# Kernel tuning notes

Hardware: AMD Instinct MI355X
Metric: run time of the kernel (lower is better)

The kernel has to match this reference:

```python
import jax, jax.numpy as jnp
import numpy as np

# Config constants (match init_kwargs)
V, E, DQ, DM, S = 50257, 256, 128, 256, 8192
WLOC, KR, KW, O = 64, 8, 4, 256
DECAY = 0.99
B, T = 8, 32


def setup_inputs() -> dict:
    key = jax.random.key(0)
    ks = jax.random.split(key, 24)
    def w(k, shape, s=0.05):
        return jax.random.normal(k, shape, jnp.float32) * s
    return {
        "input_ids": jax.random.randint(ks[0], (B, T), 0, V, dtype=jnp.int32),
        "embedding": w(ks[1], (V, E), 0.02),
        "Wq": w(ks[2], (E, DQ)), "Wk": w(ks[3], (E, DQ)), "Wv": w(ks[4], (E, E)),
        "Wr": w(ks[5], (3 * E, DM)),
        "Wx0": w(ks[6], (2 * E, 2 * E)), "Wh0": w(ks[7], (E, 2 * E)), "b0": jnp.zeros((2 * E,), jnp.float32),
        "Wx1": w(ks[8], (E, 2 * E)), "Wh1": w(ks[9], (E, 2 * E)), "b1": jnp.zeros((2 * E,), jnp.float32),
        "Wx2": w(ks[10], (E, 2 * E)), "Wh2": w(ks[11], (E, 2 * E)), "b2": jnp.zeros((2 * E,), jnp.float32),
        "Ww": w(ks[12], (3 * E, DM)), "Wwq": w(ks[13], (3 * E, DM)),
        "ln_g": jnp.ones((3 * E,), jnp.float32), "ln_b": jnp.zeros((3 * E,), jnp.float32),
        "Wout": w(ks[14], (3 * E, O)), "bout": jnp.zeros((O,), jnp.float32),
        "memory_init": jnp.zeros((B, S, DM), jnp.float32),
    }


def _tier(x, s, Wx, Wh, b):
    # GRU-style gated update: pre -> (update gate z, candidate h)
    pre = x @ Wx + s @ Wh + b
    z, h = jnp.split(pre, 2, axis=-1)
    z = jax.nn.sigmoid(z)
    return (1.0 - z) * s + z * jnp.tanh(h)


def reference(input_ids, embedding, Wq, Wk, Wv, Wr,
              Wx0, Wh0, b0, Wx1, Wh1, b1, Wx2, Wh2, b2,
              Ww, Wwq, ln_g, ln_b, Wout, bout, memory_init):
    Bsz = input_ids.shape[0]
    inv_sq_dq = 1.0 / np.sqrt(DQ).astype(np.float32)
    inv_sq_dm = 1.0 / np.sqrt(DM).astype(np.float32)

    def step(carry, tok):
        mem, rema, lw, s0, s1, s2, buf, t = carry
        e = embedding[tok]                                    # [B,E]
        # --- local sliding-window attention (circular buffer + validity mask) ---
        valid = jnp.minimum(t, WLOC)
        q = e @ Wq                                            # [B,DQ]
        k = buf @ Wk                                          # [B,W,DQ]
        v = buf @ Wv                                          # [B,W,E]
        sc = jnp.einsum('bwd,bd->bw', k, q) * inv_sq_dq
        mask = jnp.arange(WLOC) < valid
        sc = jnp.where(mask[None, :], sc, -1e9)
        attn = jax.nn.softmax(sc, axis=-1)
        local_read = jnp.einsum('bw,bwd->bd', attn, v) * (valid > 0).astype(e.dtype)
        buf = buf.at[:, t % WLOC, :].set(e)                   # update buffer
        # --- sparse top-k router read from memory bank ---
        u = jnp.concatenate([e, s0, s2], axis=-1)             # [B,3E]
        qm = u @ Wr                                           # [B,DM]
        rsc = jnp.einsum('bsd,bd->bs', mem, qm) * inv_sq_dm - 0.1 * rema
        rvals, ridx = jax.lax.top_k(rsc, KR)
        alpha = jax.nn.softmax(rvals, axis=-1)                # [B,KR]
        rows = jnp.take_along_axis(mem, ridx[:, :, None], axis=1)
        r = jnp.einsum('bk,bkd->bd', alpha, rows)             # [B,DM]
        rema = DECAY * rema
        rema = jax.vmap(lambda rr, ii, aa: rr.at[ii].add(aa))(rema, ridx, alpha)
        # --- hierarchical tier update (period-gated) ---
        x0 = jnp.concatenate([e, r + local_read], axis=-1)
        s0n = _tier(x0, s0, Wx0, Wh0, b0)                     # period 1
        s1n = jnp.where(t % 2 == 0, _tier(s0n, s1, Wx1, Wh1, b1), s1)
        s2n = jnp.where(t % 4 == 0, _tier(s1n, s2, Wx2, Wh2, b2), s2)
        # --- memory writer: gated scatter write to top-k stale/underused slots ---
        u2 = jnp.concatenate([s0n, s2n, r], axis=-1)          # [B,3E]
        wvec = jnp.tanh(u2 @ Ww)                              # [B,DM]
        qw = u2 @ Wwq
        tf = t.astype(jnp.float32)
        stale = (tf - lw.astype(jnp.float32)) / (tf + 1.0)
        under = 1.0 / (1.0 + rema)
        wsc = jnp.einsum('bsd,bd->bs', mem, qw) * inv_sq_dm + 0.5 * stale + 0.5 * under
        gvals, widx = jax.lax.top_k(wsc, KW)
        g = jax.nn.sigmoid(gvals)[..., None]                  # [B,KW,1]
        old = jnp.take_along_axis(mem, widx[:, :, None], axis=1)
        newrows = (1.0 - g) * old + g * wvec[:, None, :]
        mem = jax.vmap(lambda m, i, vv: m.at[i].set(vv))(mem, widx, newrows)
        lw = jax.vmap(lambda l, i: l.at[i].set(t))(lw, widx)
        # --- layernorm over concatenated tiers + output head ---
        cat = jnp.concatenate([s0n, s1n, s2n], axis=-1)       # [B,3E]
        mu = cat.mean(-1, keepdims=True)
        var = ((cat - mu) ** 2).mean(-1, keepdims=True)
        nrm = (cat - mu) / jnp.sqrt(var + 1e-5) * ln_g + ln_b
        logits = nrm @ Wout + bout
        return (mem, rema, lw, s0n, s1n, s2n, buf, t + 1), logits

    init = (memory_init,
            jnp.zeros((Bsz, S), jnp.float32),
            jnp.zeros((Bsz, S), jnp.int32),
            jnp.zeros((Bsz, E), jnp.float32),
            jnp.zeros((Bsz, E), jnp.float32),
            jnp.zeros((Bsz, E), jnp.float32),
            jnp.zeros((Bsz, WLOC, E), jnp.float32),
            jnp.int32(0))
    _, logits = jax.lax.scan(step, init, input_ids.T)         # [T,B,O]
    return jnp.transpose(logits, (1, 0, 2))                   # [B,T,O]
```

## Files before the change

### kernel.cpp

```cpp
#include <hip/hip_runtime.h>
#include <math.h>

static constexpr int Bz = 8;
static constexpr int Tn = 32;
static constexpr int Ed = 256;
static constexpr int Dm = 256;
static constexpr int Sn = 8192;
static constexpr int Kr = 8;
static constexpr int Kw = 4;

#define INV_SQ_DQ 0.08838834764831845f
#define INV_SQ_DM 0.0625f
#define DECAYF    0.99f
#define LD4(p) (*reinterpret_cast<const float4*>(p))

__device__ __forceinline__ float wsc_formula(float aw, float tf, float lwf, float inv_t1, float rm) {
  return aw + 0.5f * ((tf - lwf) * inv_t1) + 0.5f / (1.f + rm);
}

template<int RA, int RB>
__device__ __forceinline__ void gseg(const float* __restrict__ W, const float* __restrict__ xv,
                                     int j4, float4& acc) {
#pragma unroll 16
  for (int r = RA; r < RB; ++r) {
    float4 w4 = LD4(W + (size_t)r * 512 + j4);
    float x = xv[r];
    acc.x += x * w4.x; acc.y += x * w4.y; acc.z += x * w4.z; acc.w += x * w4.w;
  }
}

__device__ __forceinline__ void first_untouched(const int* __restrict__ flagb, int K, int tid,
                                                int* un, int* ucnt, int* wcnt) {
  if (tid == 0) *ucnt = 0;
  __syncthreads();
  for (int chunk = 0; chunk < 2; ++chunk) {
    int idx = chunk * 256 + tid;
    bool pred = (flagb[idx] == 0);
    unsigned long long m = __ballot(pred);
    int lane = tid & 63, wv = tid >> 6;
    if (lane == 0) wcnt[wv] = __popcll(m);
    __syncthreads();
    int pre = *ucnt;
    for (int w2 = 0; w2 < wv; ++w2) pre += wcnt[w2];
    pre += __popcll(m & ((1ull << lane) - 1ull));
    if (pred && pre < K) un[pre] = idx;
    __syncthreads();
    if (tid == 0) {
      int tot = wcnt[0] + wcnt[1] + wcnt[2] + wcnt[3];
      int nc = *ucnt + tot; *ucnt = nc > K ? K : nc;
    }
    __syncthreads();
  }
}

__device__ __forceinline__ void topk_sel(const float* __restrict__ cv, const int* __restrict__ cs,
                                         int n, int K, int tid, float* tv, int* ts,
                                         float* rv, int* ri) {
  float v0 = (tid < n) ? cv[tid] : -INFINITY;        int s0 = (tid < n) ? cs[tid] : 0x7fffffff;
  float v1 = (tid + 256 < n) ? cv[tid + 256] : -INFINITY; int s1 = (tid + 256 < n) ? cs[tid + 256] : 0x7fffffff;
  float v2 = (tid + 512 < n) ? cv[tid + 512] : -INFINITY; int s2 = (tid + 512 < n) ? cs[tid + 512] : 0x7fffffff;
  int lane = tid & 63, wv = tid >> 6;
  for (int k = 0; k < K; ++k) {
    float bv = v0; int bs = s0;
    if (v1 > bv || (v1 == bv && s1 < bs)) { bv = v1; bs = s1; }
    if (v2 > bv || (v2 == bv && s2 < bs)) { bv = v2; bs = s2; }
    for (int off = 32; off; off >>= 1) {
      float ov = __shfl_down(bv, off); int os = __shfl_down(bs, off);
      if (ov > bv || (ov == bv && os < bs)) { bv = ov; bs = os; }
    }
    if (lane == 0) { rv[wv] = bv; ri[wv] = bs; }
    __syncthreads();
    if (tid == 0) {
      float gv = rv[0]; int gs = ri[0];
      for (int w = 1; w < 4; ++w) if (rv[w] > gv || (rv[w] == gv && ri[w] < gs)) { gv = rv[w]; gs = ri[w]; }
      tv[k] = gv; ts[k] = gs;
    }
    __syncthreads();
    int gs = ts[k];
    if (s0 == gs) v0 = -INFINITY;
    if (s1 == gs) v1 = -INFINITY;
    if (s2 == gs) v2 = -INFINITY;
  }
}

__global__ __launch_bounds__(256) void k_pre1(
    const int* __restrict__ ids, const float* __restrict__ emb,
    const float* __restrict__ Wk, const float* __restrict__ Wq, const float* __restrict__ Wv,
    float* __restrict__ Kpre, float* __restrict__ qpre, float* __restrict__ Vpre) {
  int bt = blockIdx.x, tid = threadIdx.x;
  int b = bt >> 5, tt = bt & 31;
  __shared__ float el[256];
  el[tid] = emb[(size_t)ids[b * Tn + tt] * Ed + tid];
  __syncthreads();
  float a = 0.f;
  if (tid < 128) {
#pragma unroll 8
    for (int d = 0; d < 256; ++d) a += el[d] * Wk[d * 128 + tid];
    Kpre[(size_t)bt * 128 + tid] = a;
  } else {
    int j = tid - 128;
#pragma unroll 8
    for (int d = 0; d < 256; ++d) a += el[d] * Wq[d * 128 + j];
    qpre[(size_t)bt * 128 + j] = a;
  }
  float av = 0.f;
#pragma unroll 8
  for (int d = 0; d < 256; ++d) av += el[d] * Wv[d * 256 + tid];
  Vpre[(size_t)bt * 256 + tid] = av;
}

__global__ __launch_bounds__(256) void k_pre2(
    const float* __restrict__ Kpre, const float* __restrict__ qpre, const float* __restrict__ Vpre,
    float* __restrict__ lrpre) {
  int bt = blockIdx.x, tid = threadIdx.x;
  int b = bt >> 5, tt = bt & 31;
  if (tt == 0) { lrpre[(size_t)bt * 256 + tid] = 0.f; return; }
  __shared__ float ql[128];
  __shared__ float scl[32];
  __shared__ float attn_s[64];
  if (tid < 128) ql[tid] = qpre[(size_t)bt * 128 + tid];
  __syncthreads();
  int w = tid >> 3, i = tid & 7;
  float p = 0.f;
  if (w < tt) {
    const float* kp = Kpre + (size_t)(b * Tn + w) * 128 + i * 16;
    const float* qp = ql + i * 16;
#pragma unroll
    for (int d = 0; d < 16; ++d) p += kp[d] * qp[d];
  }
  p += __shfl_xor(p, 1); p += __shfl_xor(p, 2); p += __shfl_xor(p, 4);
  if (i == 0 && w < tt) scl[w] = p * INV_SQ_DQ;
  __syncthreads();
  if (tid < 64) {
    float val = (tid < tt) ? scl[tid] : -INFINITY;
    float m = val;
    for (int off = 32; off; off >>= 1) m = fmaxf(m, __shfl_xor(m, off));
    float ex = (tid < tt) ? expf(val - m) : 0.f;
    float sm = ex;
    for (int off = 32; off; off >>= 1) sm += __shfl_xor(sm, off);
    attn_s[tid] = ex / sm;
  }
  __syncthreads();
  float acc = 0.f;
  for (int w2 = 0; w2 < tt; ++w2) acc += attn_s[w2] * Vpre[(size_t)(b * Tn + w2) * 256 + tid];
  lrpre[(size_t)bt * 256 + tid] = acc;
}

__global__ __launch_bounds__(256) void k_read(
    const float* __restrict__ rsc, float* __restrict__ rema, const float* __restrict__ mem,
    float* __restrict__ rbuf, int* __restrict__ flagI, int* __restrict__ listI,
    int* __restrict__ countI) {
  int b = blockIdx.x, tid = threadIdx.x;
  int* flagb = flagI + b * Sn;
  int* listb = listI + b * 512;
  const float* rscb = rsc + (size_t)b * Sn;
  float* remab = rema + (size_t)b * Sn;
  int cnt = countI[b];
  __shared__ float cv[544]; __shared__ int cs[544];
  __shared__ int un[8]; __shared__ int ucnt; __shared__ int wcnt[4];
  __shared__ float rv[4]; __shared__ int ri[4];
  __shared__ float tv[Kr]; __shared__ int ts[Kr];
  for (int i = tid; i < cnt; i += 256) { int s = listb[i]; cv[i] = rscb[s]; cs[i] = s; }
  first_untouched(flagb, Kr, tid, un, &ucnt, wcnt);
  if (tid < Kr) { cv[cnt + tid] = 0.f; cs[cnt + tid] = un[tid]; }
  __syncthreads();
  topk_sel(cv, cs, cnt + Kr, Kr, tid, tv, ts, rv, ri);
  float mx = tv[0];
  float ssum = 0.f;
#pragma unroll
  for (int k = 0; k < Kr; ++k) ssum += expf(tv[k] - mx);
  float inv = 1.f / ssum;
  float racc = 0.f;
#pragma unroll
  for (int k = 0; k < Kr; ++k)
    racc += (expf(tv[k] - mx) * inv) * mem[((size_t)b * Sn + ts[k]) * 256 + tid];
  rbuf[b * 256 + tid] = racc;
  for (int i = tid; i < cnt; i += 256) remab[listb[i]] *= DECAYF;
  __syncthreads();
  if (tid < Kr) {
    int s = ts[tid];
    remab[s] += expf(tv[tid] - mx) * inv;
    if (flagb[s] == 0) { flagb[s] = 1; int pos = atomicAdd(&countI[b], 1); listb[pos] = s; }
  }
}

__global__ __launch_bounds__(512) void k_tiers(
    const int* __restrict__ ids, const float* __restrict__ emb,
    const float* __restrict__ lrpre, const float* __restrict__ rbuf,
    const float* __restrict__ Wx0, const float* __restrict__ Wh0, const float* __restrict__ b0v,
    const float* __restrict__ Wx1, const float* __restrict__ Wh1, const float* __restrict__ b1v,
    const float* __restrict__ Wx2, const float* __restrict__ Wh2, const float* __restrict__ b2v,
    float* __restrict__ s0g, float* __restrict__ s1g, float* __restrict__ s2g, int t) {
  int b = blockIdx.x, tid = threadIdx.x;
  __shared__ float xa[768];
  __shared__ float snl[256];
  __shared__ float sold[256];
  __shared__ float part[4][512];
  if (tid < 256) {
    xa[tid] = emb[(size_t)ids[b * Tn + t] * Ed + tid];
    xa[512 + tid] = s0g[b * 256 + tid];
  } else {
    int d = tid - 256;
    xa[256 + d] = rbuf[b * 256 + d] + lrpre[(size_t)(b * Tn + t) * 256 + d];
  }
  __syncthreads();
  int quar = tid >> 7;
  int j4 = (tid & 127) << 2;
  {
    float4 acc = {0.f, 0.f, 0.f, 0.f};
    if (quar == 0)      gseg<0, 192>(Wx0, xa, j4, acc);
    else if (quar == 1) gseg<192, 384>(Wx0, xa, j4, acc);
    else if (quar == 2) { gseg<384, 512>(Wx0, xa, j4, acc); gseg<0, 64>(Wh0, xa + 512, j4, acc); }
    else                gseg<64, 256>(Wh0, xa + 512, j4, acc);
    *reinterpret_cast<float4*>(&part[quar][j4]) = acc;
  }
  __syncthreads();
  if (tid < 256) {
    float z = part[0][tid] + part[1][tid] + part[2][tid] + part[3][tid] + b0v[tid];
    float h = part[0][tid + 256] + part[1][tid + 256] + part[2][tid + 256] + part[3][tid + 256] + b0v[tid + 256];
    float zz = 1.f / (1.f + expf(-z));
    float ns = (1.f - zz) * xa[512 + tid] + zz * tanhf(h);
    s0g[b * 256 + tid] = ns; snl[tid] = ns;
  }
  __syncthreads();
  if ((t & 1) == 0) {
    if (tid < 256) sold[tid] = s1g[b * 256 + tid];
    __syncthreads();
    {
      float4 acc = {0.f, 0.f, 0.f, 0.f};
      if (quar == 0)      gseg<0, 128>(Wx1, snl, j4, acc);
      else if (quar == 1) gseg<128, 256>(Wx1, snl, j4, acc);
      else if (quar == 2) gseg<0, 128>(Wh1, sold, j4, acc);
      else                gseg<128, 256>(Wh1, sold, j4, acc);
      *reinterpret_cast<float4*>(&part[quar][j4]) = acc;
    }
    __syncthreads();
    if (tid < 256) {
      float z = part[0][tid] + part[1][tid] + part[2][tid] + part[3][tid] + b1v[tid];
      float h = part[0][tid + 256] + part[1][tid + 256] + part[2][tid + 256] + part[3][tid + 256] + b1v[tid + 256];
      float zz = 1.f / (1.f + expf(-z));
      float ns = (1.f - zz) * sold[tid] + zz * tanhf(h);
      s1g[b * 256 + tid] = ns;
    }
    __syncthreads();
    if ((t & 3) == 0) {
      if (tid < 256) { snl[tid] = s1g[b * 256 + tid]; sold[tid] = s2g[b * 256 + tid]; }
      __syncthreads();
      {
        float4 acc = {0.f, 0.f, 0.f, 0.f};
        if (quar == 0)      gseg<0, 128>(Wx2, snl, j4, acc);
        else if (quar == 1) gseg<128, 256>(Wx2, snl, j4, acc);
        else if (quar == 2) gseg<0, 128>(Wh2, sold, j4, acc);
        else                gseg<128, 256>(Wh2, sold, j4, acc);
        *reinterpret_cast<float4*>(&part[quar][j4]) = acc;
      }
      __syncthreads();
      if (tid < 256) {
        float z = part[0][tid] + part[1][tid] + part[2][tid] + part[3][tid] + b2v[tid];
        float h = part[0][tid + 256] + part[1][tid + 256] + part[2][tid + 256] + part[3][tid + 256] + b2v[tid + 256];
        float zz = 1.f / (1.f + expf(-z));
        s2g[b * 256 + tid] = (1.f - zz) * sold[tid] + zz * tanhf(h);
      }
    }
  }
}

__global__ __launch_bounds__(256) void k_midp(
    const int* __restrict__ ids, const float* __restrict__ emb,
    const float* __restrict__ Wr, const float* __restrict__ Wwq, const float* __restrict__ Ww,
    const float* __restrict__ s0g, const float* __restrict__ s1g, const float* __restrict__ s2g,
    const float* __restrict__ rbuf,
    const float* __restrict__ lng, const float* __restrict__ lnb,
    float* __restrict__ qmP, float* __restrict__ qwP, float* __restrict__ wvP,
    float* __restrict__ nrm, int t) {
  int wg = blockIdx.x, tid = threadIdx.x;
  if (wg < 96) {
    int m = wg >> 5;
    int r = wg & 31;
    int b = r >> 2, q = r & 3;
    if (m == 0 && t + 1 >= Tn) return;
    if (m != 0 && t >= Tn - 1) return;
    __shared__ float xl[192];
    if (tid < 192) {
      int row = q * 192 + tid;
      float val;
      if (m == 0) {
        if (row < 256) val = emb[(size_t)ids[b * Tn + t + 1] * Ed + row];
        else if (row < 512) val = s0g[b * 256 + row - 256];
        else val = s2g[b * 256 + row - 512];
      } else {
        if (row < 256) val = s0g[b * 256 + row];
        else if (row < 512) val = s2g[b * 256 + row - 256];
        else val = rbuf[b * 256 + row - 512];
      }
      xl[tid] = (m < 2) ? val * INV_SQ_DM : val;
    }
    __syncthreads();
    const float* W = (m == 0) ? Wr : (m == 1) ? Wwq : Ww;
    W += (size_t)(q * 192) * 256;
    float a = 0.f;
#pragma unroll 16
    for (int i = 0; i < 192; ++i) a += xl[i] * W[(size_t)i * 256 + tid];
    float* dst = (m == 0) ? qmP : (m == 1) ? qwP : wvP;
    dst[q * 2048 + b * 256 + tid] = a;
  } else {
    int b = wg - 96;
    __shared__ float red[4];
    float c0 = s0g[b * 256 + tid], c1 = s1g[b * 256 + tid], c2 = s2g[b * 256 + tid];
    float partl = c0 + c1 + c2;
    int lane = tid & 63, wv = tid >> 6;
    for (int off = 32; off; off >>= 1) partl += __shfl_down(partl, off);
    if (lane == 0) red[wv] = partl;
    __syncthreads();
    float mu = (red[0] + red[1] + red[2] + red[3]) * (1.f / 768.f);
    __syncthreads();
    float d0 = c0 - mu, d1 = c1 - mu, d2 = c2 - mu;
    float p2 = d0 * d0 + d1 * d1 + d2 * d2;
    for (int off = 32; off; off >>= 1) p2 += __shfl_down(p2, off);
    if (lane == 0) red[wv] = p2;
    __syncthreads();
    float var = (red[0] + red[1] + red[2] + red[3]) * (1.f / 768.f);
    float rstd = 1.f / sqrtf(var + 1e-5f);
    nrm[b * 768 + tid]       = d0 * rstd * lng[tid]       + lnb[tid];
    nrm[b * 768 + tid + 256] = d1 * rstd * lng[tid + 256] + lnb[tid + 256];
    nrm[b * 768 + tid + 512] = d2 * rstd * lng[tid + 512] + lnb[tid + 512];
  }
}

__global__ __launch_bounds__(256) void k_logits(
    const float* __restrict__ nrm, const float* __restrict__ Wout, const float* __restrict__ boutp,
    float* __restrict__ out, int t) {
  int wg = blockIdx.x, tid = threadIdx.x;
  int b = wg >> 2, c = wg & 3;
  __shared__ float lnl[192];
  if (tid < 192) lnl[tid] = nrm[b * 768 + c * 192 + tid];
  __syncthreads();
  float a = (c == 0) ? boutp[tid] : 0.f;
#pragma unroll 16
  for (int i = 0; i < 192; ++i) a += lnl[i] * Wout[(size_t)(c * 192 + i) * 256 + tid];
  atomicAdd(out + ((size_t)b * Tn + t) * 256 + tid, a);
}

__global__ __launch_bounds__(256) void k_scores(
    const float* __restrict__ mem, const float* __restrict__ qmP, const float* __restrict__ qwP,
    const float* __restrict__ rema, const int* __restrict__ lwI,
    const int* __restrict__ listI, const int* __restrict__ countI,
    float* __restrict__ rsc, float* __restrict__ wsc, int t) {
  int wg = blockIdx.x, tid = threadIdx.x;
  int b = wg >> 2, partq = wg & 3;
  int lane = tid & 63, wv = tid >> 6;
  int cnt = countI[b];
  float4 qm4 = {0, 0, 0, 0}, qw4 = {0, 0, 0, 0};
#pragma unroll
  for (int q = 0; q < 4; ++q) {
    float4 a = LD4(qmP + q * 2048 + b * 256 + lane * 4);
    float4 c = LD4(qwP + q * 2048 + b * 256 + lane * 4);
    qm4.x += a.x; qm4.y += a.y; qm4.z += a.z; qm4.w += a.w;
    qw4.x += c.x; qw4.y += c.y; qw4.z += c.z; qw4.w += c.w;
  }
  float tf = (float)t;
  float inv_t1 = 1.f / (tf + 1.f);
  for (int i = partq * 4 + wv; i < cnt; i += 16) {
    int s = listI[b * 512 + i];
    float4 m4 = LD4(mem + ((size_t)b * Sn + s) * 256 + lane * 4);
    float ar = m4.x * qm4.x + m4.y * qm4.y + m4.z * qm4.z + m4.w * qm4.w;
    float aw = m4.x * qw4.x + m4.y * qw4.y + m4.z * qw4.z + m4.w * qw4.w;
    for (int off = 32; off; off >>= 1) { ar += __shfl_down(ar, off); aw += __shfl_down(aw, off); }
    if (lane == 0) {
      float rm = rema[(size_t)b * Sn + s];
      float lwf = (float)lwI[b * Sn + s];
      rsc[(size_t)b * Sn + s] = ar - 0.1f * rm;
      wsc[(size_t)b * Sn + s] = wsc_formula(aw, tf, lwf, inv_t1, rm);
    }
  }
}

__global__ __launch_bounds__(256) void k_write(
    const float* __restrict__ wsc, float* __restrict__ mem,
    const float* __restrict__ wvP, const float* __restrict__ qmP,
    const float* __restrict__ rema, int* __restrict__ lwI,
    float* __restrict__ rsc, int* __restrict__ flagI, int* __restrict__ listI,
    int* __restrict__ countI, int t) {
  int b = blockIdx.x, tid = threadIdx.x;
  int* flagb = flagI + b * Sn;
  int* listb = listI + b * 512;
  const float* wscb = wsc + (size_t)b * Sn;
  float* rscb = rsc + (size_t)b * Sn;
  const float* remab = rema + (size_t)b * Sn;
  int cnt = countI[b];
  __shared__ float cv[544]; __shared__ int cs[544];
  __shared__ int un[8]; __shared__ int ucnt; __shared__ int wcnt[4];
  __shared__ float rv[4]; __shared__ int ri[4];
  __shared__ float tv[Kw]; __shared__ int ts[Kw];
  for (int i = tid; i < cnt; i += 256) { int s = listb[i]; cv[i] = wscb[s]; cs[i] = s; }
  first_untouched(flagb, Kw, tid, un, &ucnt, wcnt);
  float tf = (float)t;
  float inv_t1 = 1.f / (tf + 1.f);
  if (tid < Kw) { cv[cnt + tid] = wsc_formula(0.f, tf, 0.f, inv_t1, 0.f); cs[cnt + tid] = un[tid]; }
  __syncthreads();
  topk_sel(cv, cs, cnt + Kw, Kw, tid, tv, ts, rv, ri);
  float wvv = tanhf(wvP[0 * 2048 + b * 256 + tid] + wvP[1 * 2048 + b * 256 + tid] +
                    wvP[2 * 2048 + b * 256 + tid] + wvP[3 * 2048 + b * 256 + tid]);
  float qv = qmP[0 * 2048 + b * 256 + tid] + qmP[1 * 2048 + b * 256 + tid] +
             qmP[2 * 2048 + b * 256 + tid] + qmP[3 * 2048 + b * 256 + tid];
  int lane = tid & 63, wv = tid >> 6;
  for (int k = 0; k < Kw; ++k) {
    int s = ts[k];
    float g = 1.f / (1.f + expf(-tv[k]));
    float* row = mem + ((size_t)b * Sn + s) * 256;
    float nv = (1.f - g) * row[tid] + g * wvv;
    row[tid] = nv;
    float p = nv * qv;
    for (int off = 32; off; off >>= 1) p += __shfl_down(p, off);
    if (lane == 0) rv[wv] = p;
    __syncthreads();
    if (tid == 0) {
      rscb[s] = (rv[0] + rv[1] + rv[2] + rv[3]) - 0.1f * remab[s];
      lwI[b * Sn + s] = t;
    }
    __syncthreads();
  }
  if (tid < Kw) {
    int s = ts[tid];
    if (flagb[s] == 0) { flagb[s] = 1; int pos = atomicAdd(&countI[b], 1); listb[pos] = s; }
  }
}

extern "C" void kernel_launch(void* const* d_in, const int* in_sizes, int n_in,
                              void* d_out, int out_size, void* d_ws, size_t ws_size,
                              hipStream_t stream) {
  (void)in_sizes; (void)n_in; (void)out_size; (void)ws_size;
  const int*   ids   = (const int*)d_in[0];
  const float* emb   = (const float*)d_in[1];
  const float* Wq    = (const float*)d_in[2];
  const float* Wk    = (const float*)d_in[3];
  const float* Wv    = (const float*)d_in[4];
  const float* Wr    = (const float*)d_in[5];
  const float* Wx0   = (const float*)d_in[6];
  const float* Wh0   = (const float*)d_in[7];
  const float* b0p   = (const float*)d_in[8];
  const float* Wx1   = (const float*)d_in[9];
  const float* Wh1   = (const float*)d_in[10];
  const float* b1p   = (const float*)d_in[11];
  const float* Wx2   = (const float*)d_in[12];
  const float* Wh2   = (const float*)d_in[13];
  const float* b2p   = (const float*)d_in[14];
  const float* Ww    = (const float*)d_in[15];
  const float* Wwq   = (const float*)d_in[16];
  const float* lng   = (const float*)d_in[17];
  const float* lnb   = (const float*)d_in[18];
  const float* Wout  = (const float*)d_in[19];
  const float* boutp = (const float*)d_in[20];
  float* mem = (float*)d_in[21];

  float* ws = (float*)d_ws;
  size_t off = 0;
  float* rsc  = ws + off; off += (size_t)Bz * Sn;
  float* wsc  = ws + off; off += (size_t)Bz * Sn;
  float* rema = ws + off; off += (size_t)Bz * Sn;
  int*   lwI   = (int*)(ws + off); off += (size_t)Bz * Sn;
  int*   flagI = (int*)(ws + off); off += (size_t)Bz * Sn;
  int*   listI = (int*)(ws + off); off += (size_t)Bz * 512;
  int*   countI = (int*)(ws + off); off += 64;
  float* qmP  = ws + off; off += 4 * 2048;
  float* qwP  = ws + off; off += 4 * 2048;
  float* wvP  = ws + off; off += 4 * 2048;
  float* rbuf = ws + off; off += Bz * Ed;
  float* s0g  = ws + off; off += Bz * Ed;
  float* s1g  = ws + off; off += Bz * Ed;
  float* s2g  = ws + off; off += Bz * Ed;
  float* nrm  = ws + off; off += Bz * 768;
  float* Kpre = ws + off; off += (size_t)Bz * Tn * 128;
  float* qpre = ws + off; off += (size_t)Bz * Tn * 128;
  float* Vpre = ws + off; off += (size_t)Bz * Tn * 256;
  float* lrpre = ws + off; off += (size_t)Bz * Tn * 256;

  hipMemsetAsync(d_ws, 0, off * sizeof(float), stream);
  hipMemsetAsync(d_out, 0, (size_t)Bz * Tn * 256 * sizeof(float), stream);

  k_pre1<<<256, 256, 0, stream>>>(ids, emb, Wk, Wq, Wv, Kpre, qpre, Vpre);
  k_pre2<<<256, 256, 0, stream>>>(Kpre, qpre, Vpre, lrpre);

  for (int t = 0; t < Tn; ++t) {
    k_read<<<8, 256, 0, stream>>>(rsc, rema, mem, rbuf, flagI, listI, countI);
    k_tiers<<<8, 512, 0, stream>>>(ids, emb, lrpre, rbuf,
                                   Wx0, Wh0, b0p, Wx1, Wh1, b1p, Wx2, Wh2, b2p,
                                   s0g, s1g, s2g, t);
    k_midp<<<104, 256, 0, stream>>>(ids, emb, Wr, Wwq, Ww, s0g, s1g, s2g, rbuf,
                                    lng, lnb, qmP, qwP, wvP, nrm, t);
    k_logits<<<32, 256, 0, stream>>>(nrm, Wout, boutp, (float*)d_out, t);
    if (t < Tn - 1) {
      k_scores<<<32, 256, 0, stream>>>(mem, qmP, qwP, rema, lwI, listI, countI, rsc, wsc, t);
      k_write<<<8, 256, 0, stream>>>(wsc, mem, wvP, qmP, rema, lwI, rsc, flagI, listI, countI, t);
    }
  }
}
```

Baseline: 2.321 ms.

## Fuse per-step kernels into a persistent megakernel with grid barriers

Replaces the roughly 190 per-timestep kernel launches with one persistent kernel of 64 blocks that steps through phases separated by atomic-counter grid barriers. The tier GEMVs, projections and logits are split across more blocks with K-chunk partials reduced in a follow-up phase, and write plus next read are merged into one phase. Tier updates for s1 and s2 are gated on t parity, and the memset of d_out and several buffers is dropped. This targets launch overhead and latency on a serial recurrence, at the cost of spin-wait barriers that rely on all 64 blocks being co-resident.

```diff
diff --git a/kernel.cpp b/kernel.cpp
--- a/kernel.cpp
+++ b/kernel.cpp
@@ -1,85 +1,368 @@
 #include <hip/hip_runtime.h>
 #include <math.h>
 
-static constexpr int Bz = 8;
-static constexpr int Tn = 32;
-static constexpr int Ed = 256;
-static constexpr int Dm = 256;
-static constexpr int Sn = 8192;
-static constexpr int Kr = 8;
-static constexpr int Kw = 4;
-
+static constexpr int Bz = 8, Tn = 32, Sn = 8192, Kr = 8, Kw = 4;
 #define INV_SQ_DQ 0.08838834764831845f
 #define INV_SQ_DM 0.0625f
 #define DECAYF    0.99f
+#define NBLK      64
 #define LD4(p) (*reinterpret_cast<const float4*>(p))
 
-__device__ __forceinline__ float wsc_formula(float aw, float tf, float lwf, float inv_t1, float rm) {
-  return aw + 0.5f * ((tf - lwf) * inv_t1) + 0.5f / (1.f + rm);
-}
-
-template<int RA, int RB>
-__device__ __forceinline__ void gseg(const float* __restrict__ W, const float* __restrict__ xv,
-                                     int j4, float4& acc) {
-#pragma unroll 16
-  for (int r = RA; r < RB; ++r) {
-    float4 w4 = LD4(W + (size_t)r * 512 + j4);
-    float x = xv[r];
-    acc.x += x * w4.x; acc.y += x * w4.y; acc.z += x * w4.z; acc.w += x * w4.w;
-  }
-}
-
-__device__ __forceinline__ void first_untouched(const int* __restrict__ flagb, int K, int tid,
-                                                int* un, int* ucnt, int* wcnt) {
-  if (tid == 0) *ucnt = 0;
+struct MA {
+  const int* ids; const float* emb;
+  const float* Wr;
+  const float* Wx0; const float* Wh0; const float* b0;
+  const float* Wx1; const float* Wh1; const float* b1;
+  const float* Wx2; const float* Wh2; const float* b2;
+  const float* Ww; const float* Wwq; const float* lng; const float* lnb;
+  const float* Wout; const float* bout;
+  float* mem; float* out;
+  float* rsc; float* wsc; float* rema; int* lw; int* flag; int* list; int* cnt;
+  int* bar;
+  float* s0; float* s1; float* s2; float* rbuf; float* x0; float* nrm;
+  float* qmv; float* qwv; float* wvv;
+  float* pT; float* pP; float* pL;
+  const float* lrpre;
+};
+
+struct Sh {
+  float* xs; float* cv; int* cs; float* tv; int* ts; float* rv; int* ri;
+  int* un; int* uc; int* wc;
+};
+
+__device__ __forceinline__ void gbar(int* cnt, int ep) {
+  __syncthreads();
+  if (threadIdx.x == 0) {
+    __threadfence();
+    atomicAdd(cnt, 1);
+    int tgt = ep * NBLK;
+    while (__hip_atomic_load(cnt, __ATOMIC_RELAXED, __HIP_MEMORY_SCOPE_AGENT) < tgt)
+      __builtin_amdgcn_s_sleep(8);
+    __threadfence();
+  }
+  __syncthreads();
+}
+
+__device__ void first_untouched(const int* __restrict__ flagb, int K, int tid, const Sh& sh) {
+  if (tid == 0) *sh.uc = 0;
   __syncthreads();
   for (int chunk = 0; chunk < 2; ++chunk) {
     int idx = chunk * 256 + tid;
     bool pred = (flagb[idx] == 0);
     unsigned long long m = __ballot(pred);
     int lane = tid & 63, wv = tid >> 6;
-    if (lane == 0) wcnt[wv] = __popcll(m);
-    __syncthreads();
-    int pre = *ucnt;
-    for (int w2 = 0; w2 < wv; ++w2) pre += wcnt[w2];
+    if (lane == 0) sh.wc[wv] = __popcll(m);
+    __syncthreads();
+    int pre = *sh.uc;
+    for (int w2 = 0; w2 < wv; ++w2) pre += sh.wc[w2];
     pre += __popcll(m & ((1ull << lane) - 1ull));
-    if (pred && pre < K) un[pre] = idx;
+    if (pred && pre < K) sh.un[pre] = idx;
     __syncthreads();
     if (tid == 0) {
-      int tot = wcnt[0] + wcnt[1] + wcnt[2] + wcnt[3];
-      int nc = *ucnt + tot; *ucnt = nc > K ? K : nc;
-    }
-    __syncthreads();
-  }
-}
-
-__device__ __forceinline__ void topk_sel(const float* __restrict__ cv, const int* __restrict__ cs,
-                                         int n, int K, int tid, float* tv, int* ts,
-                                         float* rv, int* ri) {
-  float v0 = (tid < n) ? cv[tid] : -INFINITY;        int s0 = (tid < n) ? cs[tid] : 0x7fffffff;
-  float v1 = (tid + 256 < n) ? cv[tid + 256] : -INFINITY; int s1 = (tid + 256 < n) ? cs[tid + 256] : 0x7fffffff;
-  float v2 = (tid + 512 < n) ? cv[tid + 512] : -INFINITY; int s2 = (tid + 512 < n) ? cs[tid + 512] : 0x7fffffff;
+      int tot = sh.wc[0] + sh.wc[1] + sh.wc[2] + sh.wc[3];
+      int nc = *sh.uc + tot; *sh.uc = nc > K ? K : nc;
+    }
+    __syncthreads();
+  }
+}
+
+__device__ void topk_sel(const Sh& sh, int n, int K, int tid) {
+  float v0 = (tid < n) ? sh.cv[tid] : -INFINITY;
+  int s0 = (tid < n) ? sh.cs[tid] : 0x7fffffff;
+  float v1 = (tid + 256 < n) ? sh.cv[tid + 256] : -INFINITY;
+  int s1 = (tid + 256 < n) ? sh.cs[tid + 256] : 0x7fffffff;
   int lane = tid & 63, wv = tid >> 6;
   for (int k = 0; k < K; ++k) {
     float bv = v0; int bs = s0;
     if (v1 > bv || (v1 == bv && s1 < bs)) { bv = v1; bs = s1; }
-    if (v2 > bv || (v2 == bv && s2 < bs)) { bv = v2; bs = s2; }
     for (int off = 32; off; off >>= 1) {
       float ov = __shfl_down(bv, off); int os = __shfl_down(bs, off);
       if (ov > bv || (ov == bv && os < bs)) { bv = ov; bs = os; }
     }
-    if (lane == 0) { rv[wv] = bv; ri[wv] = bs; }
+    if (lane == 0) { sh.rv[wv] = bv; sh.ri[wv] = bs; }
     __syncthreads();
     if (tid == 0) {
-      float gv = rv[0]; int gs = ri[0];
-      for (int w = 1; w < 4; ++w) if (rv[w] > gv || (rv[w] == gv && ri[w] < gs)) { gv = rv[w]; gs = ri[w]; }
-      tv[k] = gv; ts[k] = gs;
-    }
-    __syncthreads();
-    int gs = ts[k];
+      float gv = sh.rv[0]; int gs = sh.ri[0];
+      for (int w = 1; w < 4; ++w)
+        if (sh.rv[w] > gv || (sh.rv[w] == gv && sh.ri[w] < gs)) { gv = sh.rv[w]; gs = sh.ri[w]; }
+      sh.tv[k] = gv; sh.ts[k] = gs;
+    }
+    __syncthreads();
+    int gs = sh.ts[k];
     if (s0 == gs) v0 = -INFINITY;
     if (s1 == gs) v1 = -INFINITY;
-    if (s2 == gs) v2 = -INFINITY;
+  }
+}
+
+__device__ void tier_part(const float* __restrict__ WA, int RA,
+                          const float* __restrict__ WB, int RB,
+                          const float* __restrict__ xA, const float* __restrict__ xB,
+                          float* __restrict__ part, int K8, int blk, int tid, float* xs) {
+  int kc = blk >> 1, jh = blk & 1, base = kc * K8;
+  for (int i = tid; i < K8 * 8; i += 256) {
+    int rr = i >> 3, b = i & 7, r = base + rr;
+    xs[rr * 8 + b] = (r < RA) ? xA[b * RA + r] : xB[b * RB + r - RA];
+  }
+  __syncthreads();
+  int j = jh * 256 + tid;
+  float acc[8] = {0, 0, 0, 0, 0, 0, 0, 0};
+#pragma unroll 8
+  for (int rr = 0; rr < K8; ++rr) {
+    int r = base + rr;
+    float w = (r < RA) ? WA[(size_t)r * 512 + j] : WB[(size_t)(r - RA) * 512 + j];
+    float4 xlo = LD4(xs + rr * 8), xhi = LD4(xs + rr * 8 + 4);
+    acc[0] += xlo.x * w; acc[1] += xlo.y * w; acc[2] += xlo.z * w; acc[3] += xlo.w * w;
+    acc[4] += xhi.x * w; acc[5] += xhi.y * w; acc[6] += xhi.z * w; acc[7] += xhi.w * w;
+  }
+#pragma unroll
+  for (int b = 0; b < 8; ++b) part[(size_t)(kc * 8 + b) * 512 + j] = acc[b];
+}
+
+__device__ void tier_fin(const float* __restrict__ part, const float* __restrict__ bias,
+                         float* __restrict__ sg, int b, int tid) {
+  float z = bias[tid], h = bias[tid + 256];
+#pragma unroll
+  for (int kc = 0; kc < 8; ++kc) {
+    z += part[(size_t)(kc * 8 + b) * 512 + tid];
+    h += part[(size_t)(kc * 8 + b) * 512 + tid + 256];
+  }
+  float zz = 1.f / (1.f + expf(-z));
+  float so = sg[b * 256 + tid];
+  sg[b * 256 + tid] = (1.f - zz) * so + zz * tanhf(h);
+}
+
+__device__ void proj_part(const MA& a, int m, int kc, int t, int tid, float* xs) {
+  const float* W = (m == 0) ? a.Wr : (m == 1) ? a.Wwq : a.Ww;
+  for (int i = tid; i < 768; i += 256) {
+    int rr = i >> 3, b = i & 7, r = kc * 96 + rr;
+    float v;
+    if (m == 0) {
+      if (r < 256) v = a.emb[(size_t)a.ids[b * Tn + t + 1] * 256 + r];
+      else if (r < 512) v = a.s0[b * 256 + r - 256];
+      else v = a.s2[b * 256 + r - 512];
+      v *= INV_SQ_DM;
+    } else {
+      if (r < 256) v = a.s0[b * 256 + r];
+      else if (r < 512) v = a.s2[b * 256 + r - 256];
+      else v = a.rbuf[b * 256 + r - 512];
+      if (m == 1) v *= INV_SQ_DM;
+    }
+    xs[rr * 8 + b] = v;
+  }
+  __syncthreads();
+  float acc[8] = {0, 0, 0, 0, 0, 0, 0, 0};
+  const float* Wp = W + (size_t)(kc * 96) * 256 + tid;
+#pragma unroll 8
+  for (int rr = 0; rr < 96; ++rr) {
+    float w = Wp[(size_t)rr * 256];
+    float4 xlo = LD4(xs + rr * 8), xhi = LD4(xs + rr * 8 + 4);
+    acc[0] += xlo.x * w; acc[1] += xlo.y * w; acc[2] += xlo.z * w; acc[3] += xlo.w * w;
+    acc[4] += xhi.x * w; acc[5] += xhi.y * w; acc[6] += xhi.z * w; acc[7] += xhi.w * w;
+  }
+#pragma unroll
+  for (int b = 0; b < 8; ++b) a.pP[(size_t)((m * 8 + kc) * 8 + b) * 256 + tid] = acc[b];
+}
+
+__device__ void proj_fin(const MA& a, int m, int b, int tid) {
+  float s = 0.f;
+#pragma unroll
+  for (int kc = 0; kc < 8; ++kc) s += a.pP[(size_t)((m * 8 + kc) * 8 + b) * 256 + tid];
+  if (m == 0) a.qmv[b * 256 + tid] = s;
+  else if (m == 1) a.qwv[b * 256 + tid] = s;
+  else a.wvv[b * 256 + tid] = tanhf(s);
+}
+
+__device__ void ln_phase(const MA& a, int b, int tid, float* red) {
+  float c0 = a.s0[b * 256 + tid], c1 = a.s1[b * 256 + tid], c2 = a.s2[b * 256 + tid];
+  float part = c0 + c1 + c2;
+  int lane = tid & 63, wv = tid >> 6;
+  for (int off = 32; off; off >>= 1) part += __shfl_down(part, off);
+  if (lane == 0) red[wv] = part;
+  __syncthreads();
+  float mu = (red[0] + red[1] + red[2] + red[3]) * (1.f / 768.f);
+  __syncthreads();
+  float d0 = c0 - mu, d1 = c1 - mu, d2 = c2 - mu;
+  float p2 = d0 * d0 + d1 * d1 + d2 * d2;
+  for (int off = 32; off; off >>= 1) p2 += __shfl_down(p2, off);
+  if (lane == 0) red[wv] = p2;
+  __syncthreads();
+  float var = (red[0] + red[1] + red[2] + red[3]) * (1.f / 768.f);
+  float rstd = 1.f / sqrtf(var + 1e-5f);
+  a.nrm[b * 768 + tid]       = d0 * rstd * a.lng[tid]       + a.lnb[tid];
+  a.nrm[b * 768 + tid + 256] = d1 * rstd * a.lng[tid + 256] + a.lnb[tid + 256];
+  a.nrm[b * 768 + tid + 512] = d2 * rstd * a.lng[tid + 512] + a.lnb[tid + 512];
+}
+
+__device__ void logits_part(const MA& a, int kc, int tid, float* xs) {
+  for (int i = tid; i < 768; i += 256) {
+    int rr = i >> 3, b = i & 7;
+    xs[rr * 8 + b] = a.nrm[b * 768 + kc * 96 + rr];
+  }
+  __syncthreads();
+  float acc[8] = {0, 0, 0, 0, 0, 0, 0, 0};
+  const float* Wp = a.Wout + (size_t)(kc * 96) * 256 + tid;
+#pragma unroll 8
+  for (int rr = 0; rr < 96; ++rr) {
+    float w = Wp[(size_t)rr * 256];
+    float4 xlo = LD4(xs + rr * 8), xhi = LD4(xs + rr * 8 + 4);
+    acc[0] += xlo.x * w; acc[1] += xlo.y * w; acc[2] += xlo.z * w; acc[3] += xlo.w * w;
+    acc[4] += xhi.x * w; acc[5] += xhi.y * w; acc[6] += xhi.z * w; acc[7] += xhi.w * w;
+  }
+#pragma unroll
+  for (int b = 0; b < 8; ++b) a.pL[(size_t)(kc * 8 + b) * 256 + tid] = acc[b];
+}
+
+__device__ void logits_fin(const MA& a, int b, int t, int tid) {
+  float s = a.bout[tid];
+#pragma unroll
+  for (int kc = 0; kc < 8; ++kc) s += a.pL[(size_t)(kc * 8 + b) * 256 + tid];
+  a.out[((size_t)b * Tn + t) * 256 + tid] = s;
+}
+
+__device__ void scores_phase(const MA& a, int sb, int t, int tid) {
+  int b = sb / 6, part = sb % 6;
+  int lane = tid & 63, wv = tid >> 6;
+  int cnt = a.cnt[b];
+  const int* listb = a.list + b * 512;
+  float4 qm4 = LD4(a.qmv + b * 256 + lane * 4);
+  float4 qw4 = LD4(a.qwv + b * 256 + lane * 4);
+  float tf = (float)t, inv_t1 = 1.f / (tf + 1.f);
+  for (int i = part * 4 + wv; i < cnt; i += 24) {
+    int s = listb[i];
+    float4 m4 = LD4(a.mem + ((size_t)b * Sn + s) * 256 + lane * 4);
+    float ar = m4.x * qm4.x + m4.y * qm4.y + m4.z * qm4.z + m4.w * qm4.w;
+    float aw = m4.x * qw4.x + m4.y * qw4.y + m4.z * qw4.z + m4.w * qw4.w;
+    for (int off = 32; off; off >>= 1) { ar += __shfl_down(ar, off); aw += __shfl_down(aw, off); }
+    if (lane == 0) {
+      float rm = a.rema[(size_t)b * Sn + s];
+      a.rsc[(size_t)b * Sn + s] = ar - 0.1f * rm;
+      a.wsc[(size_t)b * Sn + s] = aw + 0.5f * ((tf - (float)a.lw[b * Sn + s]) * inv_t1) + 0.5f / (1.f + rm);
+    }
+  }
+}
+
+__device__ void read_phase(const MA& a, const Sh& sh, int b, int tN, int tid) {
+  int* flagb = a.flag + b * Sn;
+  int* listb = a.list + b * 512;
+  const float* rscb = a.rsc + (size_t)b * Sn;
+  float* remab = a.rema + (size_t)b * Sn;
+  int cnt = a.cnt[b];
+  for (int i = tid; i < cnt; i += 256) { int s = listb[i]; sh.cv[i] = rscb[s]; sh.cs[i] = s; }
+  first_untouched(flagb, Kr, tid, sh);
+  if (tid < Kr) { sh.cv[cnt + tid] = 0.f; sh.cs[cnt + tid] = sh.un[tid]; }
+  __syncthreads();
+  topk_sel(sh, cnt + Kr, Kr, tid);
+  float mx = sh.tv[0], ssum = 0.f;
+#pragma unroll
+  for (int k = 0; k < Kr; ++k) ssum += expf(sh.tv[k] - mx);
+  float inv = 1.f / ssum;
+  float racc = 0.f;
+#pragma unroll
+  for (int k = 0; k < Kr; ++k)
+    racc += (expf(sh.tv[k] - mx) * inv) * a.mem[((size_t)b * Sn + sh.ts[k]) * 256 + tid];
+  a.rbuf[b * 256 + tid] = racc;
+  a.x0[b * 512 + tid] = a.emb[(size_t)a.ids[b * Tn + tN] * 256 + tid];
+  a.x0[b * 512 + 256 + tid] = racc + a.lrpre[((size_t)b * Tn + tN) * 256 + tid];
+  for (int i = tid; i < cnt; i += 256) remab[listb[i]] *= DECAYF;
+  __syncthreads();
+  if (tid < Kr) remab[sh.ts[tid]] += expf(sh.tv[tid] - mx) * inv;
+  __syncthreads();
+  if (tid == 0) {
+    int c = cnt;
+    for (int k = 0; k < Kr; ++k) {
+      int s = sh.ts[k];
+      if (flagb[s] == 0) { flagb[s] = 1; listb[c++] = s; }
+    }
+    a.cnt[b] = c;
+  }
+  __syncthreads();
+}
+
+__device__ void write_read(const MA& a, const Sh& sh, int b, int t, int tid) {
+  int* flagb = a.flag + b * Sn;
+  int* listb = a.list + b * 512;
+  const float* wscb = a.wsc + (size_t)b * Sn;
+  float* rscb = a.rsc + (size_t)b * Sn;
+  float* remab = a.rema + (size_t)b * Sn;
+  int cnt = a.cnt[b];
+  for (int i = tid; i < cnt; i += 256) { int s = listb[i]; sh.cv[i] = wscb[s]; sh.cs[i] = s; }
+  first_untouched(flagb, Kw, tid, sh);
+  float tf = (float)t, inv_t1 = 1.f / (tf + 1.f);
+  if (tid < Kw) { sh.cv[cnt + tid] = 0.5f * (tf * inv_t1) + 0.5f; sh.cs[cnt + tid] = sh.un[tid]; }
+  __syncthreads();
+  topk_sel(sh, cnt + Kw, Kw, tid);
+  float wvvv = a.wvv[b * 256 + tid];
+  float qv = a.qmv[b * 256 + tid];
+  int lane = tid & 63, wv = tid >> 6;
+  for (int k = 0; k < Kw; ++k) {
+    int s = sh.ts[k];
+    float g = 1.f / (1.f + expf(-sh.tv[k]));
+    float* row = a.mem + ((size_t)b * Sn + s) * 256;
+    float nv = (1.f - g) * row[tid] + g * wvvv;
+    row[tid] = nv;
+    float p = nv * qv;
+    for (int off = 32; off; off >>= 1) p += __shfl_down(p, off);
+    if (lane == 0) sh.rv[wv] = p;
+    __syncthreads();
+    if (tid == 0) {
+      rscb[s] = (sh.rv[0] + sh.rv[1] + sh.rv[2] + sh.rv[3]) - 0.1f * remab[s];
+      a.lw[b * Sn + s] = t;
+    }
+    __syncthreads();
+  }
+  if (tid == 0) {
+    int c = cnt;
+    for (int k = 0; k < Kw; ++k) {
+      int s = sh.ts[k];
+      if (flagb[s] == 0) { flagb[s] = 1; listb[c++] = s; }
+    }
+    a.cnt[b] = c;
+  }
+  __syncthreads();
+  read_phase(a, sh, b, t + 1, tid);
+}
+
+__global__ __launch_bounds__(256, 1) void mega(MA a) {
+  __shared__ float xsS[96 * 8];
+  __shared__ float cvS[544]; __shared__ int csS[544];
+  __shared__ float tvS[8];   __shared__ int tsS[8];
+  __shared__ float rvS[4];   __shared__ int riS[4];
+  __shared__ int unS[8];     __shared__ int ucS; __shared__ int wcS[4];
+  Sh sh{xsS, cvS, csS, tvS, tsS, rvS, riS, unS, &ucS, wcS};
+  int blk = blockIdx.x, tid = threadIdx.x;
+  int ep = 0;
+
+  if (blk < 8) read_phase(a, sh, blk, 0, tid);
+  gbar(a.bar, ++ep);
+
+  for (int t = 0; t < Tn; ++t) {
+    if (blk < 16) tier_part(a.Wx0, 512, a.Wh0, 256, a.x0, a.s0, a.pT, 96, blk, tid, xsS);
+    gbar(a.bar, ++ep);
+    if (blk < 8) tier_fin(a.pT, a.b0, a.s0, blk, tid);
+    gbar(a.bar, ++ep);
+    if ((t & 1) == 0) {
+      if (blk < 16) tier_part(a.Wx1, 256, a.Wh1, 256, a.s0, a.s1, a.pT, 64, blk, tid, xsS);
+      gbar(a.bar, ++ep);
+      if (blk < 8) tier_fin(a.pT, a.b1, a.s1, blk, tid);
+      gbar(a.bar, ++ep);
+      if ((t & 3) == 0) {
+        if (blk < 16) tier_part(a.Wx2, 256, a.Wh2, 256, a.s1, a.s2, a.pT, 64, blk, tid, xsS);
+        gbar(a.bar, ++ep);
+        if (blk < 8) tier_fin(a.pT, a.b2, a.s2, blk, tid);
+        gbar(a.bar, ++ep);
+      }
+    }
+    if (blk < 24) { if (t < Tn - 1) proj_part(a, blk >> 3, blk & 7, t, tid, xsS); }
+    else if (blk < 32) ln_phase(a, blk - 24, tid, rvS);
+    gbar(a.bar, ++ep);
+    if (blk < 24) { if (t < Tn - 1) proj_fin(a, blk >> 3, blk & 7, tid); }
+    else if (blk < 32) logits_part(a, blk - 24, tid, xsS);
+    gbar(a.bar, ++ep);
+    if (blk < 8) logits_fin(a, blk, t, tid);
+    else if (blk < 56) { if (t < Tn - 1) scores_phase(a, blk - 8, t, tid); }
+    gbar(a.bar, ++ep);
+    if (t < Tn - 1 && blk < 8) write_read(a, sh, blk, t, tid);
+    gbar(a.bar, ++ep);
   }
 }
 
@@ -90,7 +373,7 @@
   int bt = blockIdx.x, tid = threadIdx.x;
   int b = bt >> 5, tt = bt & 31;
   __shared__ float el[256];
-  el[tid] = emb[(size_t)ids[b * Tn + tt] * Ed + tid];
+  el[tid] = emb[(size_t)ids[b * Tn + tt] * 256 + tid];
   __syncthreads();
   float a = 0.f;
   if (tid < 128) {
@@ -146,352 +429,57 @@
   lrpre[(size_t)bt * 256 + tid] = acc;
 }
 
-__global__ __launch_bounds__(256) void k_read(
-    const float* __restrict__ rsc, float* __restrict__ rema, const float* __restrict__ mem,
-    float* __restrict__ rbuf, int* __restrict__ flagI, int* __restrict__ listI,
-    int* __restrict__ countI) {
-  int b = blockIdx.x, tid = threadIdx.x;
-  int* flagb = flagI + b * Sn;
-  int* listb = listI + b * 512;
-  const float* rscb = rsc + (size_t)b * Sn;
-  float* remab = rema + (size_t)b * Sn;
-  int cnt = countI[b];
-  __shared__ float cv[544]; __shared__ int cs[544];
-  __shared__ int un[8]; __shared__ int ucnt; __shared__ int wcnt[4];
-  __shared__ float rv[4]; __shared__ int ri[4];
-  __shared__ float tv[Kr]; __shared__ int ts[Kr];
-  for (int i = tid; i < cnt; i += 256) { int s = listb[i]; cv[i] = rscb[s]; cs[i] = s; }
-  first_untouched(flagb, Kr, tid, un, &ucnt, wcnt);
-  if (tid < Kr) { cv[cnt + tid] = 0.f; cs[cnt + tid] = un[tid]; }
-  __syncthreads();
-  topk_sel(cv, cs, cnt + Kr, Kr, tid, tv, ts, rv, ri);
-  float mx = tv[0];
-  float ssum = 0.f;
-#pragma unroll
-  for (int k = 0; k < Kr; ++k) ssum += expf(tv[k] - mx);
-  float inv = 1.f / ssum;
-  float racc = 0.f;
-#pragma unroll
-  for (int k = 0; k < Kr; ++k)
-    racc += (expf(tv[k] - mx) * inv) * mem[((size_t)b * Sn + ts[k]) * 256 + tid];
-  rbuf[b * 256 + tid] = racc;
-  for (int i = tid; i < cnt; i += 256) remab[listb[i]] *= DECAYF;
-  __syncthreads();
-  if (tid < Kr) {
-    int s = ts[tid];
-    remab[s] += expf(tv[tid] - mx) * inv;
-    if (flagb[s] == 0) { flagb[s] = 1; int pos = atomicAdd(&countI[b], 1); listb[pos] = s; }
-  }
-}
-
-__global__ __launch_bounds__(512) void k_tiers(
-    const int* __restrict__ ids, const float* __restrict__ emb,
-    const float* __restrict__ lrpre, const float* __restrict__ rbuf,
-    const float* __restrict__ Wx0, const float* __restrict__ Wh0, const float* __restrict__ b0v,
-    const float* __restrict__ Wx1, const float* __restrict__ Wh1, const float* __restrict__ b1v,
-    const float* __restrict__ Wx2, const float* __restrict__ Wh2, const float* __restrict__ b2v,
-    float* __restrict__ s0g, float* __restrict__ s1g, float* __restrict__ s2g, int t) {
-  int b = blockIdx.x, tid = threadIdx.x;
-  __shared__ float xa[768];
-  __shared__ float snl[256];
-  __shared__ float sold[256];
-  __shared__ float part[4][512];
-  if (tid < 256) {
-    xa[tid] = emb[(size_t)ids[b * Tn + t] * Ed + tid];
-    xa[512 + tid] = s0g[b * 256 + tid];
-  } else {
-    int d = tid - 256;
-    xa[256 + d] = rbuf[b * 256 + d] + lrpre[(size_t)(b * Tn + t) * 256 + d];
-  }
-  __syncthreads();
-  int quar = tid >> 7;
-  int j4 = (tid & 127) << 2;
-  {
-    float4 acc = {0.f, 0.f, 0.f, 0.f};
-    if (quar == 0)      gseg<0, 192>(Wx0, xa, j4, acc);
-    else if (quar == 1) gseg<192, 384>(Wx0, xa, j4, acc);
-    else if (quar == 2) { gseg<384, 512>(Wx0, xa, j4, acc); gseg<0, 64>(Wh0, xa + 512, j4, acc); }
-    else                gseg<64, 256>(Wh0, xa + 512, j4, acc);
-    *reinterpret_cast<float4*>(&part[quar][j4]) = acc;
-  }
-  __syncthreads();
-  if (tid < 256) {
-    float z = part[0][tid] + part[1][tid] + part[2][tid] + part[3][tid] + b0v[tid];
-    float h = part[0][tid + 256] + part[1][tid + 256] + part[2][tid + 256] + part[3][tid + 256] + b0v[tid + 256];
-    float zz = 1.f / (1.f + expf(-z));
-    float ns = (1.f - zz) * xa[512 + tid] + zz * tanhf(h);
-    s0g[b * 256 + tid] = ns; snl[tid] = ns;
-  }
-  __syncthreads();
-  if ((t & 1) == 0) {
-    if (tid < 256) sold[tid] = s1g[b * 256 + tid];
-    __syncthreads();
-    {
-      float4 acc = {0.f, 0.f, 0.f, 0.f};
-      if (quar == 0)      gseg<0, 128>(Wx1, snl, j4, acc);
-      else if (quar == 1) gseg<128, 256>(Wx1, snl, j4, acc);
-      else if (quar == 2) gseg<0, 128>(Wh1, sold, j4, acc);
-      else                gseg<128, 256>(Wh1, sold, j4, acc);
-      *reinterpret_cast<float4*>(&part[quar][j4]) = acc;
-    }
-    __syncthreads();
-    if (tid < 256) {
-      float z = part[0][tid] + part[1][tid] + part[2][tid] + part[3][tid] + b1v[tid];
-      float h = part[0][tid + 256] + part[1][tid + 256] + part[2][tid + 256] + part[3][tid + 256] + b1v[tid + 256];
-      float zz = 1.f / (1.f + expf(-z));
-      float ns = (1.f - zz) * sold[tid] + zz * tanhf(h);
-      s1g[b * 256 + tid] = ns;
-    }
-    __syncthreads();
-    if ((t & 3) == 0) {
-      if (tid < 256) { snl[tid] = s1g[b * 256 + tid]; sold[tid] = s2g[b * 256 + tid]; }
-      __syncthreads();
-      {
-        float4 acc = {0.f, 0.f, 0.f, 0.f};
-        if (quar == 0)      gseg<0, 128>(Wx2, snl, j4, acc);
-        else if (quar == 1) gseg<128, 256>(Wx2, snl, j4, acc);
-        else if (quar == 2) gseg<0, 128>(Wh2, sold, j4, acc);
-        else                gseg<128, 256>(Wh2, sold, j4, acc);
-        *reinterpret_cast<float4*>(&part[quar][j4]) = acc;
-      }
-      __syncthreads();
-      if (tid < 256) {
-        float z = part[0][tid] + part[1][tid] + part[2][tid] + part[3][tid] + b2v[tid];
-        float h = part[0][tid + 256] + part[1][tid + 256] + part[2][tid + 256] + part[3][tid + 256] + b2v[tid + 256];
-        float zz = 1.f / (1.f + expf(-z));
-        s2g[b * 256 + tid] = (1.f - zz) * sold[tid] + zz * tanhf(h);
-      }
-    }
-  }
-}
-
-__global__ __launch_bounds__(256) void k_midp(
-    const int* __restrict__ ids, const float* __restrict__ emb,
-    const float* __restrict__ Wr, const float* __restrict__ Wwq, const float* __restrict__ Ww,
-    const float* __restrict__ s0g, const float* __restrict__ s1g, const float* __restrict__ s2g,
-    const float* __restrict__ rbuf,
-    const float* __restrict__ lng, const float* __restrict__ lnb,
-    float* __restrict__ qmP, float* __restrict__ qwP, float* __restrict__ wvP,
-    float* __restrict__ nrm, int t) {
-  int wg = blockIdx.x, tid = threadIdx.x;
-  if (wg < 96) {
-    int m = wg >> 5;
-    int r = wg & 31;
-    int b = r >> 2, q = r & 3;
-    if (m == 0 && t + 1 >= Tn) return;
-    if (m != 0 && t >= Tn - 1) return;
-    __shared__ float xl[192];
-    if (tid < 192) {
-      int row = q * 192 + tid;
-      float val;
-      if (m == 0) {
-        if (row < 256) val = emb[(size_t)ids[b * Tn + t + 1] * Ed + row];
-        else if (row < 512) val = s0g[b * 256 + row - 256];
-        else val = s2g[b * 256 + row - 512];
-      } else {
-        if (row < 256) val = s0g[b * 256 + row];
-        else if (row < 512) val = s2g[b * 256 + row - 256];
-        else val = rbuf[b * 256 + row - 512];
-      }
-      xl[tid] = (m < 2) ? val * INV_SQ_DM : val;
-    }
-    __syncthreads();
-    const float* W = (m == 0) ? Wr : (m == 1) ? Wwq : Ww;
-    W += (size_t)(q * 192) * 256;
-    float a = 0.f;
-#pragma unroll 16
-    for (int i = 0; i < 192; ++i) a += xl[i] * W[(size_t)i * 256 + tid];
-    float* dst = (m == 0) ? qmP : (m == 1) ? qwP : wvP;
-    dst[q * 2048 + b * 256 + tid] = a;
-  } else {
-    int b = wg - 96;
-    __shared__ float red[4];
-    float c0 = s0g[b * 256 + tid], c1 = s1g[b * 256 + tid], c2 = s2g[b * 256 + tid];
-    float partl = c0 + c1 + c2;
-    int lane = tid & 63, wv = tid >> 6;
-    for (int off = 32; off; off >>= 1) partl += __shfl_down(partl, off);
-    if (lane == 0) red[wv] = partl;
-    __syncthreads();
-    float mu = (red[0] + red[1] + red[2] + red[3]) * (1.f / 768.f);
-    __syncthreads();
-    float d0 = c0 - mu, d1 = c1 - mu, d2 = c2 - mu;
-    float p2 = d0 * d0 + d1 * d1 + d2 * d2;
-    for (int off = 32; off; off >>= 1) p2 += __shfl_down(p2, off);
-    if (lane == 0) red[wv] = p2;
-    __syncthreads();
-    float var = (red[0] + red[1] + red[2] + red[3]) * (1.f / 768.f);
-    float rstd = 1.f / sqrtf(var + 1e-5f);
-    nrm[b * 768 + tid]       = d0 * rstd * lng[tid]       + lnb[tid];
-    nrm[b * 768 + tid + 256] = d1 * rstd * lng[tid + 256] + lnb[tid + 256];
-    nrm[b * 768 + tid + 512] = d2 * rstd * lng[tid + 512] + lnb[tid + 512];
-  }
-}
-
-__global__ __launch_bounds__(256) void k_logits(
-    const float* __restrict__ nrm, const float* __restrict__ Wout, const float* __restrict__ boutp,
-    float* __restrict__ out, int t) {
-  int wg = blockIdx.x, tid = threadIdx.x;
-  int b = wg >> 2, c = wg & 3;
-  __shared__ float lnl[192];
-  if (tid < 192) lnl[tid] = nrm[b * 768 + c * 192 + tid];
-  __syncthreads();
-  float a = (c == 0) ? boutp[tid] : 0.f;
-#pragma unroll 16
-  for (int i = 0; i < 192; ++i) a += lnl[i] * Wout[(size_t)(c * 192 + i) * 256 + tid];
-  atomicAdd(out + ((size_t)b * Tn + t) * 256 + tid, a);
-}
-
-__global__ __launch_bounds__(256) void k_scores(
-    const float* __restrict__ mem, const float* __restrict__ qmP, const float* __restrict__ qwP,
-    const float* __restrict__ rema, const int* __restrict__ lwI,
-    const int* __restrict__ listI, const int* __restrict__ countI,
-    float* __restrict__ rsc, float* __restrict__ wsc, int t) {
-  int wg = blockIdx.x, tid = threadIdx.x;
-  int b = wg >> 2, partq = wg & 3;
-  int lane = tid & 63, wv = tid >> 6;
-  int cnt = countI[b];
-  float4 qm4 = {0, 0, 0, 0}, qw4 = {0, 0, 0, 0};
-#pragma unroll
-  for (int q = 0; q < 4; ++q) {
-    float4 a = LD4(qmP + q * 2048 + b * 256 + lane * 4);
-    float4 c = LD4(qwP + q * 2048 + b * 256 + lane * 4);
-    qm4.x += a.x; qm4.y += a.y; qm4.z += a.z; qm4.w += a.w;
-    qw4.x += c.x; qw4.y += c.y; qw4.z += c.z; qw4.w += c.w;
-  }
-  float tf = (float)t;
-  float inv_t1 = 1.f / (tf + 1.f);
-  for (int i = partq * 4 + wv; i < cnt; i += 16) {
-    int s = listI[b * 512 + i];
-    float4 m4 = LD4(mem + ((size_t)b * Sn + s) * 256 + lane * 4);
-    float ar = m4.x * qm4.x + m4.y * qm4.y + m4.z * qm4.z + m4.w * qm4.w;
-    float aw = m4.x * qw4.x + m4.y * qw4.y + m4.z * qw4.z + m4.w * qw4.w;
-    for (int off = 32; off; off >>= 1) { ar += __shfl_down(ar, off); aw += __shfl_down(aw, off); }
-    if (lane == 0) {
-      float rm = rema[(size_t)b * Sn + s];
-      float lwf = (float)lwI[b * Sn + s];
-      rsc[(size_t)b * Sn + s] = ar - 0.1f * rm;
-      wsc[(size_t)b * Sn + s] = wsc_formula(aw, tf, lwf, inv_t1, rm);
-    }
-  }
-}
-
-__global__ __launch_bounds__(256) void k_write(
-    const float* __restrict__ wsc, float* __restrict__ mem,
-    const float* __restrict__ wvP, const float* __restrict__ qmP,
-    const float* __restrict__ rema, int* __restrict__ lwI,
-    float* __restrict__ rsc, int* __restrict__ flagI, int* __restrict__ listI,
-    int* __restrict__ countI, int t) {
-  int b = blockIdx.x, tid = threadIdx.x;
-  int* flagb = flagI + b * Sn;
-  int* listb = listI + b * 512;
-  const float* wscb = wsc + (size_t)b * Sn;
-  float* rscb = rsc + (size_t)b * Sn;
-  const float* remab = rema + (size_t)b * Sn;
-  int cnt = countI[b];
-  __shared__ float cv[544]; __shared__ int cs[544];
-  __shared__ int un[8]; __shared__ int ucnt; __shared__ int wcnt[4];
-  __shared__ float rv[4]; __shared__ int ri[4];
-  __shared__ float tv[Kw]; __shared__ int ts[Kw];
-  for (int i = tid; i < cnt; i += 256) { int s = listb[i]; cv[i] = wscb[s]; cs[i] = s; }
-  first_untouched(flagb, Kw, tid, un, &ucnt, wcnt);
-  float tf = (float)t;
-  float inv_t1 = 1.f / (tf + 1.f);
-  if (tid < Kw) { cv[cnt + tid] = wsc_formula(0.f, tf, 0.f, inv_t1, 0.f); cs[cnt + tid] = un[tid]; }
-  __syncthreads();
-  topk_sel(cv, cs, cnt + Kw, Kw, tid, tv, ts, rv, ri);
-  float wvv = tanhf(wvP[0 * 2048 + b * 256 + tid] + wvP[1 * 2048 + b * 256 + tid] +
-                    wvP[2 * 2048 + b * 256 + tid] + wvP[3 * 2048 + b * 256 + tid]);
-  float qv = qmP[0 * 2048 + b * 256 + tid] + qmP[1 * 2048 + b * 256 + tid] +
-             qmP[2 * 2048 + b * 256 + tid] + qmP[3 * 2048 + b * 256 + tid];
-  int lane = tid & 63, wv = tid >> 6;
-  for (int k = 0; k < Kw; ++k) {
-    int s = ts[k];
-    float g = 1.f / (1.f + expf(-tv[k]));
-    float* row = mem + ((size_t)b * Sn + s) * 256;
-    float nv = (1.f - g) * row[tid] + g * wvv;
-    row[tid] = nv;
-    float p = nv * qv;
-    for (int off = 32; off; off >>= 1) p += __shfl_down(p, off);
-    if (lane == 0) rv[wv] = p;
-    __syncthreads();
-    if (tid == 0) {
-      rscb[s] = (rv[0] + rv[1] + rv[2] + rv[3]) - 0.1f * remab[s];
-      lwI[b * Sn + s] = t;
-    }
-    __syncthreads();
-  }
-  if (tid < Kw) {
-    int s = ts[tid];
-    if (flagb[s] == 0) { flagb[s] = 1; int pos = atomicAdd(&countI[b], 1); listb[pos] = s; }
-  }
-}
-
 extern "C" void kernel_launch(void* const* d_in, const int* in_sizes, int n_in,
                               void* d_out, int out_size, void* d_ws, size_t ws_size,
                               hipStream_t stream) {
   (void)in_sizes; (void)n_in; (void)out_size; (void)ws_size;
-  const int*   ids   = (const int*)d_in[0];
-  const float* emb   = (const float*)d_in[1];
-  const float* Wq    = (const float*)d_in[2];
-  const float* Wk    = (const float*)d_in[3];
-  const float* Wv    = (const float*)d_in[4];
-  const float* Wr    = (const float*)d_in[5];
-  const float* Wx0   = (const float*)d_in[6];
-  const float* Wh0   = (const float*)d_in[7];
-  const float* b0p   = (const float*)d_in[8];
-  const float* Wx1   = (const float*)d_in[9];
-  const float* Wh1   = (const float*)d_in[10];
-  const float* b1p   = (const float*)d_in[11];
-  const float* Wx2   = (const float*)d_in[12];
-  const float* Wh2   = (const float*)d_in[13];
-  const float* b2p   = (const float*)d_in[14];
-  const float* Ww    = (const float*)d_in[15];
-  const float* Wwq   = (const float*)d_in[16];
-  const float* lng   = (const float*)d_in[17];
-  const float* lnb   = (const float*)d_in[18];
-  const float* Wout  = (const float*)d_in[19];
-  const float* boutp = (const float*)d_in[20];
-  float* mem = (float*)d_in[21];
+  MA a;
+  a.ids  = (const int*)d_in[0];
+  a.emb  = (const float*)d_in[1];
+  const float* Wq = (const float*)d_in[2];
+  const float* Wk = (const float*)d_in[3];
+  const float* Wv = (const float*)d_in[4];
+  a.Wr   = (const float*)d_in[5];
+  a.Wx0  = (const float*)d_in[6];  a.Wh0 = (const float*)d_in[7];  a.b0 = (const float*)d_in[8];
+  a.Wx1  = (const float*)d_in[9];  a.Wh1 = (const float*)d_in[10]; a.b1 = (const float*)d_in[11];
+  a.Wx2  = (const float*)d_in[12]; a.Wh2 = (const float*)d_in[13]; a.b2 = (const float*)d_in[14];
+  a.Ww   = (const float*)d_in[15]; a.Wwq = (const float*)d_in[16];
+  a.lng  = (const float*)d_in[17]; a.lnb = (const float*)d_in[18];
+  a.Wout = (const float*)d_in[19]; a.bout = (const float*)d_in[20];
+  a.mem  = (float*)d_in[21];
+  a.out  = (float*)d_out;
 
   float* ws = (float*)d_ws;
-  size_t off = 0;
-  float* rsc  = ws + off; off += (size_t)Bz * Sn;
-  float* wsc  = ws + off; off += (size_t)Bz * Sn;
-  float* rema = ws + off; off += (size_t)Bz * Sn;
-  int*   lwI   = (int*)(ws + off); off += (size_t)Bz * Sn;
-  int*   flagI = (int*)(ws + off); off += (size_t)Bz * Sn;
-  int*   listI = (int*)(ws + off); off += (size_t)Bz * 512;
-  int*   countI = (int*)(ws + off); off += 64;
-  float* qmP  = ws + off; off += 4 * 2048;
-  float* qwP  = ws + off; off += 4 * 2048;
-  float* wvP  = ws + off; off += 4 * 2048;
-  float* rbuf = ws + off; off += Bz * Ed;
-  float* s0g  = ws + off; off += Bz * Ed;
-  float* s1g  = ws + off; off += Bz * Ed;
-  float* s2g  = ws + off; off += Bz * Ed;
-  float* nrm  = ws + off; off += Bz * 768;
-  float* Kpre = ws + off; off += (size_t)Bz * Tn * 128;
-  float* qpre = ws + off; off += (size_t)Bz * Tn * 128;
-  float* Vpre = ws + off; off += (size_t)Bz * Tn * 256;
-  float* lrpre = ws + off; off += (size_t)Bz * Tn * 256;
-
-  hipMemsetAsync(d_ws, 0, off * sizeof(float), stream);
-  hipMemsetAsync(d_out, 0, (size_t)Bz * Tn * 256 * sizeof(float), stream);
-
-  k_pre1<<<256, 256, 0, stream>>>(ids, emb, Wk, Wq, Wv, Kpre, qpre, Vpre);
+  size_t o = 0;
+  a.rsc  = ws + o; o += (size_t)Bz * Sn;
+  a.rema = ws + o; o += (size_t)Bz * Sn;
+  a.lw   = (int*)(ws + o); o += (size_t)Bz * Sn;
+  a.flag = (int*)(ws + o); o += (size_t)Bz * Sn;
+  a.list = (int*)(ws + o); o += (size_t)Bz * 512;
+  a.cnt  = (int*)(ws + o); o += 16;
+  a.bar  = (int*)(ws + o); o += 16;
+  a.s0   = ws + o; o += 2048;
+  a.s1   = ws + o; o += 2048;
+  a.s2   = ws + o; o += 2048;
+  size_t zero_floats = o;
+  a.wsc  = ws + o; o += (size_t)Bz * Sn;
+  a.rbuf = ws + o; o += 2048;
+  a.x0   = ws + o; o += 4096;
+  a.nrm  = ws + o; o += 6144;
+  a.qmv  = ws + o; o += 2048;
+  a.qwv  = ws + o; o += 2048;
+  a.wvv  = ws + o; o += 2048;
+  a.pT   = ws + o; o += 8 * 8 * 512;
+  a.pP   = ws + o; o += 3 * 8 * 8 * 256;
+  a.pL   = ws + o; o += 8 * 8 * 256;
+  float* Kpre  = ws + o; o += (size_t)Bz * Tn * 128;
+  float* qpre  = ws + o; o += (size_t)Bz * Tn * 128;
+  float* Vpre  = ws + o; o += (size_t)Bz * Tn * 256;
+  float* lrpre = ws + o; o += (size_t)Bz * Tn * 256;
+  a.lrpre = lrpre;
+
+  hipMemsetAsync(d_ws, 0, zero_floats * sizeof(float), stream);
+  k_pre1<<<256, 256, 0, stream>>>(a.ids, a.emb, Wk, Wq, Wv, Kpre, qpre, Vpre);
   k_pre2<<<256, 256, 0, stream>>>(Kpre, qpre, Vpre, lrpre);
-
-  for (int t = 0; t < Tn; ++t) {
-    k_read<<<8, 256, 0, stream>>>(rsc, rema, mem, rbuf, flagI, listI, countI);
-    k_tiers<<<8, 512, 0, stream>>>(ids, emb, lrpre, rbuf,
-                                   Wx0, Wh0, b0p, Wx1, Wh1, b1p, Wx2, Wh2, b2p,
-                                   s0g, s1g, s2g, t);
-    k_midp<<<104, 256, 0, stream>>>(ids, emb, Wr, Wwq, Ww, s0g, s1g, s2g, rbuf,
-                                    lng, lnb, qmP, qwP, wvP, nrm, t);
-    k_logits<<<32, 256, 0, stream>>>(nrm, Wout, boutp, (float*)d_out, t);
-    if (t < Tn - 1) {
-      k_scores<<<32, 256, 0, stream>>>(mem, qmP, qwP, rema, lwI, listI, countI, rsc, wsc, t);
-      k_write<<<8, 256, 0, stream>>>(wsc, mem, wvP, qmP, rema, lwI, rsc, flagI, listI, countI, t);
-    }
-  }
-}
+  mega<<<NBLK, 256, 0, stream>>>(a);
+}
```

Result: slower. 3.420 ms (+47.3%).
